# Kernel optimization log

Measured on AMD Instinct MI355X. Metric: run time of the kernel, lower is better.

Reference implementation:

```python
import jax, jax.numpy as jnp
import numpy as np

N, E, DIN, DH, DOUT, NG = 50000, 800000, 128, 128, 64, 128
EPS = 1e-5
SLOPE = 0.2  # PyG GATConv default negative_slope


def _gat(x, src, dst, W, a_s, a_d, b, heads, out_c, concat):
    n = x.shape[0]
    xp = (x @ W).reshape(n, heads, out_c)            # [N,H,C]
    e_src = (xp * a_s[None]).sum(-1)                  # [N,H]
    e_dst = (xp * a_d[None]).sum(-1)                  # [N,H]
    al = e_src[src] + e_dst[dst]                      # [E,H]
    al = jnp.where(al > 0, al, SLOPE * al)            # leaky_relu
    amax = jax.ops.segment_max(al, dst, num_segments=n)
    w = jnp.exp(al - amax[dst])                       # segment softmax (stable)
    den = jax.ops.segment_sum(w, dst, num_segments=n)
    msg = w[:, :, None] * xp[src]                     # [E,H,C]
    out = jax.ops.segment_sum(msg, dst, num_segments=n) / den[:, :, None]
    out = out.reshape(n, heads * out_c) if concat else out.mean(axis=1)
    return out + b


def _bn(h, g, be):
    m = h.mean(axis=0)
    v = h.var(axis=0)  # biased var, as in torch BN training mode
    return (h - m) / jnp.sqrt(v + EPS) * g + be


def setup_inputs() -> dict:
    key = jax.random.key(0)
    ks = jax.random.split(key, 12)
    x = jax.random.normal(ks[0], (N, DIN), dtype=jnp.float32)
    edge_index = jax.random.randint(ks[1], (2, E), 0, N, dtype=jnp.int64)
    graph_pool = jax.random.uniform(ks[2], (NG, N), dtype=jnp.float32) * (2.0 / N)
    s = 0.1
    return {
        "x": x, "edge_index": edge_index, "graph_pool": graph_pool,
        "W1": jax.random.normal(ks[3], (DIN, DH), dtype=jnp.float32) * s,
        "as1": jax.random.normal(ks[4], (1, DH), dtype=jnp.float32) * s,
        "ad1": jax.random.normal(ks[5], (1, DH), dtype=jnp.float32) * s,
        "b1": jnp.zeros((DH,), jnp.float32),
        "g1": jnp.ones((DH,), jnp.float32), "be1": jnp.zeros((DH,), jnp.float32),
        "W2": jax.random.normal(ks[6], (DH, DH), dtype=jnp.float32) * s,
        "as2": jax.random.normal(ks[7], (1, DH), dtype=jnp.float32) * s,
        "ad2": jax.random.normal(ks[8], (1, DH), dtype=jnp.float32) * s,
        "b2": jnp.zeros((DH,), jnp.float32),
        "g2": jnp.ones((DH,), jnp.float32), "be2": jnp.zeros((DH,), jnp.float32),
        "W3": jax.random.normal(ks[9], (DH, DOUT), dtype=jnp.float32) * s,
        "as3": jax.random.normal(ks[10], (1, DOUT), dtype=jnp.float32) * s,
        "ad3": jax.random.normal(ks[11], (1, DOUT), dtype=jnp.float32) * s,
        "b3": jnp.zeros((DOUT,), jnp.float32),
    }


def reference(x, edge_index, graph_pool,
              W1, as1, ad1, b1, g1, be1,
              W2, as2, ad2, b2, g2, be2,
              W3, as3, ad3, b3):
    n = x.shape[0]
    loops = jnp.arange(n, dtype=edge_index.dtype)  # PyG add_self_loops=True
    src = jnp.concatenate([edge_index[0], loops])
    dst = jnp.concatenate([edge_index[1], loops])
    h = _gat(x, src, dst, W1, as1, ad1, b1, 1, DH, True)
    h = jax.nn.relu(_bn(h, g1, be1))
    h = _gat(h, src, dst, W2, as2, ad2, b2, 1, DH, True)
    h = jax.nn.relu(_bn(h, g2, be2))
    h_nodes = _gat(h, src, dst, W3, as3, ad3, b3, 1, DOUT, False)
    h_pooled = graph_pool @ h_nodes  # sparse.mm == matmul mathematically
    return (h_pooled, h_nodes)
```

## Files before the change

kernel.cpp:

```cpp
#include <hip/hip_runtime.h>
#include <hip/hip_bf16.h>

#define DIN 128
#define DH  128
#define DOUT 64
#define NGR 128
#define EPSV 1e-5f
#define SLOPE 0.2f
#define BSH 7
#define NBMAX 512
#define BCAP 3584
#define POOLB 256
#define BNSPREAD 32
#define BINCH 4096

typedef __attribute__((ext_vector_type(8))) short short8;
typedef __attribute__((ext_vector_type(4))) float float4v;

__device__ __forceinline__ unsigned short f2bf(float f) {
    union { float f; unsigned int u; } v; v.f = f;
    unsigned int r = (v.u + 0x7FFFu + ((v.u >> 16) & 1u)) >> 16;
    return (unsigned short)r;
}
__device__ __forceinline__ unsigned short f2bf_f(float f) {
    return (unsigned short)((__float_as_uint(f) + 0x8000u) >> 16);
}
__device__ __forceinline__ float bf_lo(unsigned int u) { return __uint_as_float(u << 16); }
__device__ __forceinline__ float bf_hi(unsigned int u) { return __uint_as_float(u & 0xFFFF0000u); }

__device__ __forceinline__ void pack_one(const float* W, unsigned short* PW, int cout, int t) {
    int lane = t & 63;
    int ks   = (t >> 6) & 3;
    int nt   = t >> 8;
    int nn   = nt * 16 + (lane & 15);
    int k0   = ks * 32 + (lane >> 4) * 8;
    unsigned int pk[4];
#pragma unroll
    for (int p = 0; p < 4; ++p) {
        unsigned short lo = f2bf(W[(k0 + 2 * p) * cout + nn]);
        unsigned short hi = f2bf(W[(k0 + 2 * p + 1) * cout + nn]);
        pk[p] = ((unsigned int)hi << 16) | lo;
    }
    *(uint4*)&PW[(size_t)t * 8] = make_uint4(pk[0], pk[1], pk[2], pk[3]);
}

__global__ __launch_bounds__(256) void front_a_kernel(
    const int* __restrict__ ei, int* __restrict__ bucket_cnt, int2* __restrict__ binned,
    int E, int T, int nb, int binBlocks,
    const float* __restrict__ W1, unsigned short* __restrict__ PW1,
    const float* __restrict__ W2, unsigned short* __restrict__ PW2,
    const float* __restrict__ W3, unsigned short* __restrict__ PW3,
    const float* __restrict__ GP, unsigned short* __restrict__ GPB, int n)
{
    int blk = (int)blockIdx.x;
    if (blk >= binBlocks + 20) {
        size_t t = (size_t)(blk - binBlocks - 20) * 256 + threadIdx.x;
        size_t base = t * 32;
        size_t tot = (size_t)NGR * (size_t)n;
        if (base >= tot) return;
        if (base + 32 <= tot) {
            const float* src = GP + base;
            unsigned short* dst = GPB + base;
#pragma unroll
            for (int q2 = 0; q2 < 4; ++q2) {
                float4 a = *(const float4*)&src[q2 * 8];
                float4 b = *(const float4*)&src[q2 * 8 + 4];
                uint4 o;
                o.x = ((unsigned int)f2bf_f(a.y) << 16) | f2bf_f(a.x);
                o.y = ((unsigned int)f2bf_f(a.w) << 16) | f2bf_f(a.z);
                o.z = ((unsigned int)f2bf_f(b.y) << 16) | f2bf_f(b.x);
                o.w = ((unsigned int)f2bf_f(b.w) << 16) | f2bf_f(b.z);
                *(uint4*)&dst[q2 * 8] = o;
            }
        } else {
            for (size_t k = base; k < tot; ++k) GPB[k] = f2bf_f(GP[k]);
        }
        return;
    }
    if (blk >= binBlocks) {
        int t = (blk - binBlocks) * 256 + (int)threadIdx.x;
        if (t < 2048)      pack_one(W1, PW1, 128, t);
        else if (t < 4096) pack_one(W2, PW2, 128, t - 2048);
        else if (t < 5120) pack_one(W3, PW3, 64,  t - 4096);
        return;
    }
    __shared__ int hist[NBMAX], base[NBMAX], cur[NBMAX];
    for (int i = threadIdx.x; i < nb; i += 256) hist[i] = 0;
    __syncthreads();
    int start = blk * BINCH;
    int endc  = start + BINCH; if (endc > T) endc = T;
    for (int e = start + threadIdx.x; e < endc; e += 256) {
        int d = (e < E) ? ei[E + e] : (e - E);
        atomicAdd(&hist[d >> BSH], 1);
    }
    __syncthreads();
    for (int i = threadIdx.x; i < nb; i += 256) {
        int h = hist[i];
        cur[i] = 0;
        if (h) base[i] = atomicAdd(&bucket_cnt[i], h);
    }
    __syncthreads();
    for (int e = start + threadIdx.x; e < endc; e += 256) {
        int s, d;
        if (e < E) { s = ei[e]; d = ei[E + e]; }
        else       { s = e - E; d = s; }
        int b = d >> BSH;
        int off = atomicAdd(&cur[b], 1);
        binned[(size_t)b * BCAP + base[b] + off] = make_int2(s, d);
    }
}

template <int COUT, int BNIN>
__device__ __forceinline__ void gemm_es_body(
    unsigned short* Xs, float* sSc, float* sSh, int row0,
    const void* __restrict__ Xv, const unsigned short* __restrict__ PW,
    const float* __restrict__ a_s, const float* __restrict__ a_d,
    const float* __restrict__ bnsum, const float* __restrict__ g,
    const float* __restrict__ be, float invn,
    unsigned short* __restrict__ XPB, float* __restrict__ e_src, float* __restrict__ e_dst, int n)
{
    constexpr int NT = COUT / 16;
    int tid = threadIdx.x;

    if constexpr (BNIN) {
        if (tid < 128) {
            float s = 0.f, q = 0.f;
#pragma unroll 4
            for (int k = 0; k < BNSPREAD; ++k) {
                s += bnsum[k * 256 + tid];
                q += bnsum[k * 256 + 128 + tid];
            }
            float mean = s * invn;
            float var  = q * invn - mean * mean;
            float sc   = g[tid] * rsqrtf(var + EPSV);
            sSc[tid] = sc;
            sSh[tid] = be[tid] - mean * sc;
        }
        __syncthreads();
        const unsigned short* H = (const unsigned short*)Xv;
        for (int i = tid; i < 64 * 16; i += 256) {
            int r  = i >> 4;
            int c8 = (i & 15) * 8;
            uint4 u = make_uint4(0, 0, 0, 0);
            if (row0 + r < n) u = *(const uint4*)&H[(size_t)(row0 + r) * 128 + c8];
            unsigned int uu[4] = {u.x, u.y, u.z, u.w};
            unsigned int out[4];
#pragma unroll
            for (int p = 0; p < 4; ++p) {
                int c = c8 + 2 * p;
                float a  = fmaxf(bf_lo(uu[p]) * sSc[c] + sSh[c], 0.f);
                float bq = fmaxf(bf_hi(uu[p]) * sSc[c + 1] + sSh[c + 1], 0.f);
                out[p] = ((unsigned int)f2bf_f(bq) << 16) | f2bf_f(a);
            }
            *(uint4*)&Xs[r * 136 + c8] = make_uint4(out[0], out[1], out[2], out[3]);
        }
    } else {
        const float* X = (const float*)Xv;
        for (int i = tid; i < 64 * 32; i += 256) {
            int r  = i >> 5;
            int k4 = (i & 31) * 4;
            float4 v = make_float4(0.f, 0.f, 0.f, 0.f);
            if (row0 + r < n) v = *(const float4*)&X[(size_t)(row0 + r) * 128 + k4];
            uint2 pk;
            pk.x = ((unsigned int)f2bf_f(v.y) << 16) | f2bf_f(v.x);
            pk.y = ((unsigned int)f2bf_f(v.w) << 16) | f2bf_f(v.z);
            *(uint2*)&Xs[r * 136 + k4] = pk;
        }
    }
    __syncthreads();

    int wv   = tid >> 6;
    int lane = tid & 63;
    int m0   = wv * 16;
    int cl   = lane & 15;
    int q    = lane >> 4;

    float4v acc[NT] = {};
#pragma unroll
    for (int ks = 0; ks < 4; ++ks) {
        short8 af = *(const short8*)&Xs[(m0 + cl) * 136 + ks * 32 + q * 8];
#pragma unroll
        for (int nt = 0; nt < NT; ++nt) {
            short8 bf = *(const short8*)&PW[(size_t)((nt * 4 + ks) * 64 + lane) * 8];
            acc[nt] = __builtin_amdgcn_mfma_f32_16x16x32_bf16(af, bf, acc[nt], 0, 0, 0);
        }
    }

    float asv[NT], adv[NT];
#pragma unroll
    for (int nt = 0; nt < NT; ++nt) {
        asv[nt] = a_s[nt * 16 + cl];
        adv[nt] = a_d[nt * 16 + cl];
    }
#pragma unroll
    for (int reg = 0; reg < 4; ++reg) {
        int m = row0 + m0 + q * 4 + reg;
        if (m >= n) continue;
        float ps = 0.f, pd = 0.f;
        size_t base = (size_t)m * COUT;
#pragma unroll
        for (int nt = 0; nt < NT; ++nt) {
            float v = acc[nt][reg];
            XPB[base + nt * 16 + cl] = f2bf_f(v);
            ps += v * asv[nt];
            pd += v * adv[nt];
        }
        ps += __shfl_xor(ps, 1); pd += __shfl_xor(pd, 1);
        ps += __shfl_xor(ps, 2); pd += __shfl_xor(pd, 2);
        ps += __shfl_xor(ps, 4); pd += __shfl_xor(pd, 4);
        ps += __shfl_xor(ps, 8); pd += __shfl_xor(pd, 8);
        if (cl == 0) {
            e_src[m] = ps;
            e_dst[m] = pd;
        }
    }
}

template <int COUT, int BNIN>
__global__ __launch_bounds__(256) void gemm_es_kernel(
    const void* __restrict__ Xv, const unsigned short* __restrict__ PW,
    const float* __restrict__ a_s, const float* __restrict__ a_d,
    const float* __restrict__ bnsum, const float* __restrict__ g,
    const float* __restrict__ be, float invn,
    unsigned short* __restrict__ XPB, float* __restrict__ e_src, float* __restrict__ e_dst, int n)
{
    __shared__ unsigned short Xs[64 * 136];
    __shared__ float sSc[128], sSh[128];
    gemm_es_body<COUT, BNIN>(Xs, sSc, sSh, blockIdx.x * 64,
                             Xv, PW, a_s, a_d, bnsum, g, be, invn, XPB, e_src, e_dst, n);
}

__global__ __launch_bounds__(256) void front_b_kernel(
    const int2* __restrict__ binned, const int* __restrict__ bucket_cnt,
    int* __restrict__ row_ptr, int* __restrict__ col_src, int n, int T, int nbcsr,
    const float* __restrict__ X, const unsigned short* __restrict__ PW,
    const float* __restrict__ a_s, const float* __restrict__ a_d,
    unsigned short* __restrict__ XPB, float* __restrict__ e_src, float* __restrict__ e_dst)
{
    __shared__ __align__(16) char smraw[64 * 136 * 2];
    int tid = threadIdx.x;

    if ((int)blockIdx.x < nbcsr) {
        int* cnt = (int*)smraw;
        int* rnk = cnt + 128;
        int* rp  = rnk + 128;
        int* sc  = rp + 128;
        int* red = sc + 128;
        int b = blockIdx.x;
        int node0 = b << BSH;
        const int2* bin = &binned[(size_t)b * BCAP];
        int nb_edges = bucket_cnt[b];

        int part = 0;
        for (int i = tid; i < b; i += 256) part += bucket_cnt[i];
        red[tid] = part;
        if (tid < 128) cnt[tid] = 0;
        __syncthreads();
#pragma unroll
        for (int s2 = 128; s2 > 0; s2 >>= 1) {
            if (tid < s2) red[tid] += red[tid + s2];
            __syncthreads();
        }
        int lo = red[0];

        for (int i = tid; i < nb_edges; i += 256)
            atomicAdd(&cnt[bin[i].y - node0], 1);
        __syncthreads();
        if (tid < 128) sc[tid] = cnt[tid];
        __syncthreads();
        for (int d2 = 1; d2 < 128; d2 <<= 1) {
            int t = 0;
            if (tid < 128 && tid >= d2) t = sc[tid - d2];
            __syncthreads();
            if (tid < 128) sc[tid] += t;
            __syncthreads();
        }
        if (tid < 128) {
            int excl = sc[tid] - cnt[tid];
            int r = lo + excl;
            rp[tid] = r;
            rnk[tid] = 0;
            int node = node0 + tid;
            if (node < n) row_ptr[node] = r;
        }
        if (b == 0 && tid == 0) row_ptr[n] = T;
        __syncthreads();
        for (int i = tid; i < nb_edges; i += 256) {
            int2 e = bin[i];
            int local = e.y - node0;
            int r = atomicAdd(&rnk[local], 1);
            col_src[rp[local] + r] = e.x;
        }
    } else {
        unsigned short* Xs = (unsigned short*)smraw;
        gemm_es_body<128, 0>(Xs, nullptr, nullptr, ((int)blockIdx.x - nbcsr) * 64,
                             X, PW, a_s, a_d, nullptr, nullptr, nullptr, 0.f,
                             XPB, e_src, e_dst, n);
    }
}

template <int COUT, int OUTBF, int BNOUT>
__global__ __launch_bounds__(256) void gat_aggregate_kernel(
    const unsigned short* __restrict__ XPB, const float* __restrict__ e_src,
    const float* __restrict__ e_dst, const int* __restrict__ row_ptr,
    const int* __restrict__ col_src, const float* __restrict__ bias,
    void* __restrict__ OUT, float* __restrict__ bnsumS, int n)
{
    __shared__ float bnsh[BNOUT ? 512 : 1];
    constexpr int GSH  = (COUT == 128) ? 4 : 3;
    constexpr int STEP = 64 >> GSH;
    constexpr int RSH  = (COUT == 128) ? 7 : 6;

    int wave = threadIdx.x >> 6;
    int lane = threadIdx.x & 63;
    int g    = lane >> GSH;
    int cl   = lane & ((1 << GSH) - 1);
    int d = blockIdx.x * 4 + wave;
    bool act = (d < n);
    if (!BNOUT && !act) return;

    int start = 0, end = 0;
    float ed = 0.f;
    if (act) {
        start = row_ptr[d];
        end   = row_ptr[d + 1];
        ed    = e_dst[d];
    }

    float denl = 0.f;
    float acc8[8] = {};

    for (int base = start; base < end; base += 64) {
        int t = base + lane;
        int s_l = 0; float w_l = 0.f;
        if (t < end) {
            s_l = col_src[t];
            float a = e_src[s_l] + ed;
            a = (a > 0.f) ? a : SLOPE * a;
            w_l = __expf(a);
        }
        denl += w_l;
        int cnt = end - base; if (cnt > 64) cnt = 64;

        int j = 0;
        for (; j + 16 <= cnt; j += 16) {
            int   r0 = __shfl(s_l, j + g);
            int   r1 = __shfl(s_l, j + STEP + g);
            float w0 = __shfl(w_l, j + g);
            float w1 = __shfl(w_l, j + STEP + g);
            uint4 u0 = ((const uint4*)(XPB + ((size_t)(unsigned)r0 << RSH)))[cl];
            uint4 u1 = ((const uint4*)(XPB + ((size_t)(unsigned)r1 << RSH)))[cl];
            int   r2, r3; float w2, w3; uint4 u2, u3;
            if (COUT == 128) {
                r2 = __shfl(s_l, j + 2 * STEP + g);
                r3 = __shfl(s_l, j + 3 * STEP + g);
                w2 = __shfl(w_l, j + 2 * STEP + g);
                w3 = __shfl(w_l, j + 3 * STEP + g);
                u2 = ((const uint4*)(XPB + ((size_t)(unsigned)r2 << RSH)))[cl];
                u3 = ((const uint4*)(XPB + ((size_t)(unsigned)r3 << RSH)))[cl];
            }
            unsigned int a0[4] = {u0.x, u0.y, u0.z, u0.w};
            unsigned int a1[4] = {u1.x, u1.y, u1.z, u1.w};
#pragma unroll
            for (int p = 0; p < 4; ++p) {
                acc8[2 * p]     += w0 * bf_lo(a0[p]);
                acc8[2 * p + 1] += w0 * bf_hi(a0[p]);
                acc8[2 * p]     += w1 * bf_lo(a1[p]);
                acc8[2 * p + 1] += w1 * bf_hi(a1[p]);
            }
            if (COUT == 128) {
                unsigned int a2[4] = {u2.x, u2.y, u2.z, u2.w};
                unsigned int a3[4] = {u3.x, u3.y, u3.z, u3.w};
#pragma unroll
                for (int p = 0; p < 4; ++p) {
                    acc8[2 * p]     += w2 * bf_lo(a2[p]);
                    acc8[2 * p + 1] += w2 * bf_hi(a2[p]);
                    acc8[2 * p]     += w3 * bf_lo(a3[p]);
                    acc8[2 * p + 1] += w3 * bf_hi(a3[p]);
                }
            }
        }
        for (; j < cnt; j += STEP) {
            int   r = __shfl(s_l, j + g);
            float w = __shfl(w_l, j + g);
            uint4 u = ((const uint4*)(XPB + ((size_t)(unsigned)r << RSH)))[cl];
            unsigned int au[4] = {u.x, u.y, u.z, u.w};
#pragma unroll
            for (int p = 0; p < 4; ++p) {
                acc8[2 * p]     += w * bf_lo(au[p]);
                acc8[2 * p + 1] += w * bf_hi(au[p]);
            }
        }
    }

#pragma unroll
    for (int off = (1 << GSH); off < 64; off <<= 1)
#pragma unroll
        for (int k = 0; k < 8; ++k) acc8[k] += __shfl_xor(acc8[k], off);

#pragma unroll
    for (int off = 1; off < 64; off <<= 1) denl += __shfl_xor(denl, off);
    float inv = 1.f / denl;

    float ox[8];
#pragma unroll
    for (int k = 0; k < 8; ++k) ox[k] = 0.f;
    if (act) {
#pragma unroll
        for (int k = 0; k < 8; ++k) ox[k] = acc8[k] * inv + bias[cl * 8 + k];
    }

    if (COUT == 128) {
        if (act && g == 0) {
            if (OUTBF) {
                unsigned int o0 = ((unsigned int)f2bf_f(ox[1]) << 16) | f2bf_f(ox[0]);
                unsigned int o1 = ((unsigned int)f2bf_f(ox[3]) << 16) | f2bf_f(ox[2]);
                unsigned int o2 = ((unsigned int)f2bf_f(ox[5]) << 16) | f2bf_f(ox[4]);
                unsigned int o3 = ((unsigned int)f2bf_f(ox[7]) << 16) | f2bf_f(ox[6]);
                ((uint4*)OUT)[(size_t)d * 16 + cl] = make_uint4(o0, o1, o2, o3);
            } else {
                ((float4*)OUT)[(size_t)d * 32 + cl * 2]     = make_float4(ox[0], ox[1], ox[2], ox[3]);
                ((float4*)OUT)[(size_t)d * 32 + cl * 2 + 1] = make_float4(ox[4], ox[5], ox[6], ox[7]);
            }
        }
        if (BNOUT) {
            if (g == 0) {
#pragma unroll
                for (int k = 0; k < 8; ++k) bnsh[wave * 128 + cl * 8 + k] = ox[k];
            }
            __syncthreads();
            if (wave == 0) {
                float s0 = 0.f, q0 = 0.f, s1 = 0.f, q1 = 0.f;
#pragma unroll
                for (int k = 0; k < 4; ++k) {
                    float v0 = bnsh[k * 128 + 2 * lane];
                    float v1 = bnsh[k * 128 + 2 * lane + 1];
                    s0 += v0; q0 += v0 * v0;
                    s1 += v1; q1 += v1 * v1;
                }
                float* dstb = &bnsumS[(blockIdx.x & (BNSPREAD - 1)) * 256];
                atomicAdd(&dstb[2 * lane],           s0);
                atomicAdd(&dstb[2 * lane + 1],       s1);
                atomicAdd(&dstb[128 + 2 * lane],     q0);
                atomicAdd(&dstb[128 + 2 * lane + 1], q1);
            }
        }
    } else {
        if (act && g == 0) {
            ((float4*)OUT)[(size_t)d * 16 + cl * 2]     = make_float4(ox[0], ox[1], ox[2], ox[3]);
            ((float4*)OUT)[(size_t)d * 16 + cl * 2 + 1] = make_float4(ox[4], ox[5], ox[6], ox[7]);
        }
    }
}

__global__ __launch_bounds__(256) void pool_mfma_kernel(
    const unsigned short* __restrict__ GPB, const float* __restrict__ HN,
    float* __restrict__ partial, int n, int nchunk)
{
    __shared__ unsigned short gp_s[128 * 136];
    __shared__ unsigned short ht_s[64 * 136];
    int tid = threadIdx.x;
    int wv = tid >> 6, lane = tid & 63, cl = lane & 15, q = lane >> 4;

    float4v acc[4][2] = {};

    for (int blk = blockIdx.x; blk < nchunk; blk += gridDim.x) {
        int k0 = blk * 128;

        for (int i = tid; i < 128 * 16; i += 256) {
            int r  = i >> 4;
            int kk = (i & 15) * 8;
            int gk = k0 + kk;
            uint4 v = make_uint4(0, 0, 0, 0);
            if (gk + 7 < n) {
                v = *(const uint4*)&GPB[(size_t)r * n + gk];
            } else if (gk < n) {
                unsigned short tmp[8];
#pragma unroll
                for (int e2 = 0; e2 < 8; ++e2)
                    tmp[e2] = (gk + e2 < n) ? GPB[(size_t)r * n + gk + e2] : 0;
                v = *(const uint4*)tmp;
            }
            *(uint4*)&gp_s[r * 136 + kk] = v;
        }
        for (int i = tid; i < 128 * 16; i += 256) {
            int k  = i >> 4;
            int c4 = (i & 15) * 4;
            int gk = k0 + k;
            float4 v = make_float4(0.f, 0.f, 0.f, 0.f);
            if (gk < n) v = *(const float4*)&HN[(size_t)gk * 64 + c4];
            ht_s[(c4 + 0) * 136 + k] = f2bf_f(v.x);
            ht_s[(c4 + 1) * 136 + k] = f2bf_f(v.y);
            ht_s[(c4 + 2) * 136 + k] = f2bf_f(v.z);
            ht_s[(c4 + 3) * 136 + k] = f2bf_f(v.w);
        }
        __syncthreads();

#pragma unroll
        for (int ks = 0; ks < 4; ++ks) {
            short8 bfr[2];
#pragma unroll
            for (int j = 0; j < 2; ++j)
                bfr[j] = *(const short8*)&gp_s[((wv * 2 + j) * 16 + cl) * 136 + ks * 32 + q * 8];
#pragma unroll
            for (int mt = 0; mt < 4; ++mt) {
                short8 af = *(const short8*)&ht_s[(mt * 16 + cl) * 136 + ks * 32 + q * 8];
#pragma unroll
                for (int j = 0; j < 2; ++j)
                    acc[mt][j] = __builtin_amdgcn_mfma_f32_16x16x32_bf16(af, bfr[j], acc[mt][j], 0, 0, 0);
            }
        }
        __syncthreads();
    }

    float* po = &partial[(size_t)blockIdx.x * (NGR * DOUT)];
#pragma unroll
    for (int mt = 0; mt < 4; ++mt) {
#pragma unroll
        for (int j = 0; j < 2; ++j) {
            int g = (wv * 2 + j) * 16 + cl;
            int c = mt * 16 + q * 4;
            *(float4*)&po[g * 64 + c] =
                make_float4(acc[mt][j][0], acc[mt][j][1], acc[mt][j][2], acc[mt][j][3]);
        }
    }
}

__global__ __launch_bounds__(256) void pool_reduce_kernel(
    const float* __restrict__ partial, float* __restrict__ OUT, int nblk)
{
    int i = blockIdx.x * 256 + threadIdx.x;
    float s0 = 0.f, s1 = 0.f, s2 = 0.f, s3 = 0.f;
    int p = 0;
    for (; p + 3 < nblk; p += 4) {
        s0 += partial[(size_t)(p + 0) * (NGR * DOUT) + i];
        s1 += partial[(size_t)(p + 1) * (NGR * DOUT) + i];
        s2 += partial[(size_t)(p + 2) * (NGR * DOUT) + i];
        s3 += partial[(size_t)(p + 3) * (NGR * DOUT) + i];
    }
    for (; p < nblk; ++p) s0 += partial[(size_t)p * (NGR * DOUT) + i];
    OUT[i] = (s0 + s1) + (s2 + s3);
}

extern "C" void kernel_launch(void* const* d_in, const int* in_sizes, int n_in,
                              void* d_out, int out_size, void* d_ws, size_t ws_size,
                              hipStream_t stream) {
    const float* x   = (const float*)d_in[0];
    const int*   ei  = (const int*)d_in[1];
    const float* gp  = (const float*)d_in[2];
    const float* W1  = (const float*)d_in[3];
    const float* as1 = (const float*)d_in[4];
    const float* ad1 = (const float*)d_in[5];
    const float* b1  = (const float*)d_in[6];
    const float* g1  = (const float*)d_in[7];
    const float* be1 = (const float*)d_in[8];
    const float* W2  = (const float*)d_in[9];
    const float* as2 = (const float*)d_in[10];
    const float* ad2 = (const float*)d_in[11];
    const float* b2  = (const float*)d_in[12];
    const float* g2  = (const float*)d_in[13];
    const float* be2 = (const float*)d_in[14];
    const float* W3  = (const float*)d_in[15];
    const float* as3 = (const float*)d_in[16];
    const float* ad3 = (const float*)d_in[17];
    const float* b3  = (const float*)d_in[18];

    const int N = in_sizes[0] / DIN;
    const int E = in_sizes[1] / 2;
    const int T = E + N;
    const int NB = (N + 127) >> BSH;

    char* ws = (char*)d_ws;
    auto take = [&](size_t bytes) {
        char* p = ws;
        ws += (bytes + 511) & ~(size_t)511;
        return p;
    };
    unsigned short* xpb = (unsigned short*)take((size_t)N * 128 * 2);
    unsigned short* h   = (unsigned short*)take((size_t)N * 128 * 2);
    unsigned short* gpb = (unsigned short*)take((size_t)NGR * N * 2);
    float* pool_s  = (float*)take((size_t)POOLB * NGR * DOUT * 4);
    float* esd     = (float*)take((size_t)2 * N * 4);
    float* e_src   = esd;
    float* e_dst   = esd + N;
    int*   row_ptr = (int*)take((size_t)(N + 1) * 4);
    int*   col_src = (int*)take((size_t)T * 4);
    int2*  binned  = (int2*)take((size_t)NB * BCAP * 8);
    int*   zero_rgn   = (int*)take((size_t)(NBMAX + 1 + 2 * BNSPREAD * 256) * 4);
    int*   bucket_cnt = zero_rgn;
    float* bnsum1     = (float*)(zero_rgn + NBMAX + 1);
    float* bnsum2     = bnsum1 + BNSPREAD * 256;
    unsigned short* pw1 = (unsigned short*)take((size_t)128 * 128 * 2);
    unsigned short* pw2 = (unsigned short*)take((size_t)128 * 128 * 2);
    unsigned short* pw3 = (unsigned short*)take((size_t)128 * 64 * 2);

    float* outp = (float*)d_out;
    float* hn   = outp + NGR * DOUT;

    hipMemsetAsync(zero_rgn, 0, (size_t)(NBMAX + 1 + 2 * BNSPREAD * 256) * 4, stream);

    const int binBlocks = (T + BINCH - 1) / BINCH;
    const int gpBlocks  = (int)(((size_t)NGR * N / 32 + 255) / 256);
    front_a_kernel<<<binBlocks + 20 + gpBlocks, 256, 0, stream>>>(
        ei, bucket_cnt, binned, E, T, NB, binBlocks,
        W1, pw1, W2, pw2, W3, pw3, gp, gpb, N);

    const int gx = (N + 63) / 64;
    const float invn = 1.f / N;

    front_b_kernel<<<NB + gx, 256, 0, stream>>>(binned, bucket_cnt, row_ptr, col_src, N, T, NB,
                                                x, pw1, as1, ad1, xpb, e_src, e_dst);

    gat_aggregate_kernel<128, 1, 1><<<(N + 3) / 4, 256, 0, stream>>>(
        xpb, e_src, e_dst, row_ptr, col_src, b1, h, bnsum1, N);

    gemm_es_kernel<128, 1><<<gx, 256, 0, stream>>>(h, pw2, as2, ad2,
        bnsum1, g1, be1, invn, xpb, e_src, e_dst, N);
    gat_aggregate_kernel<128, 1, 1><<<(N + 3) / 4, 256, 0, stream>>>(
        xpb, e_src, e_dst, row_ptr, col_src, b2, h, bnsum2, N);

    gemm_es_kernel<64, 1><<<gx, 256, 0, stream>>>(h, pw3, as3, ad3,
        bnsum2, g2, be2, invn, xpb, e_src, e_dst, N);
    gat_aggregate_kernel<64, 0, 0><<<(N + 3) / 4, 256, 0, stream>>>(
        xpb, e_src, e_dst, row_ptr, col_src, b3, hn, nullptr, N);

    const int nchunk = (N + 127) / 128;
    const int pb = nchunk < POOLB ? nchunk : POOLB;
    pool_mfma_kernel<<<pb, 256, 0, stream>>>(gpb, hn, pool_s, N, nchunk);
    pool_reduce_kernel<<<(NGR * DOUT + 255) / 256, 256, 0, stream>>>(pool_s, outp, pb);
}
```

Baseline: 330.2 us.

## Move graph_pool bf16 conversion into first aggregate kernel and register-buffer CSR edges

```diff
diff --git a/kernel.cpp b/kernel.cpp
--- a/kernel.cpp
+++ b/kernel.cpp
@@ -49,34 +49,9 @@
     int E, int T, int nb, int binBlocks,
     const float* __restrict__ W1, unsigned short* __restrict__ PW1,
     const float* __restrict__ W2, unsigned short* __restrict__ PW2,
-    const float* __restrict__ W3, unsigned short* __restrict__ PW3,
-    const float* __restrict__ GP, unsigned short* __restrict__ GPB, int n)
+    const float* __restrict__ W3, unsigned short* __restrict__ PW3)
 {
     int blk = (int)blockIdx.x;
-    if (blk >= binBlocks + 20) {
-        size_t t = (size_t)(blk - binBlocks - 20) * 256 + threadIdx.x;
-        size_t base = t * 32;
-        size_t tot = (size_t)NGR * (size_t)n;
-        if (base >= tot) return;
-        if (base + 32 <= tot) {
-            const float* src = GP + base;
-            unsigned short* dst = GPB + base;
-#pragma unroll
-            for (int q2 = 0; q2 < 4; ++q2) {
-                float4 a = *(const float4*)&src[q2 * 8];
-                float4 b = *(const float4*)&src[q2 * 8 + 4];
-                uint4 o;
-                o.x = ((unsigned int)f2bf_f(a.y) << 16) | f2bf_f(a.x);
-                o.y = ((unsigned int)f2bf_f(a.w) << 16) | f2bf_f(a.z);
-                o.z = ((unsigned int)f2bf_f(b.y) << 16) | f2bf_f(b.x);
-                o.w = ((unsigned int)f2bf_f(b.w) << 16) | f2bf_f(b.z);
-                *(uint4*)&dst[q2 * 8] = o;
-            }
-        } else {
-            for (size_t k = base; k < tot; ++k) GPB[k] = f2bf_f(GP[k]);
-        }
-        return;
-    }
     if (blk >= binBlocks) {
         int t = (blk - binBlocks) * 256 + (int)threadIdx.x;
         if (t < 2048)      pack_one(W1, PW1, 128, t);
@@ -251,6 +226,14 @@
         const int2* bin = &binned[(size_t)b * BCAP];
         int nb_edges = bucket_cnt[b];
 
+        int2 ebuf[14];
+        int cntE = 0;
+#pragma unroll
+        for (int k = 0; k < 14; ++k) {
+            int i = tid + k * 256;
+            if (i < nb_edges) { ebuf[k] = bin[i]; cntE = k + 1; }
+        }
+
         int part = 0;
         for (int i = tid; i < b; i += 256) part += bucket_cnt[i];
         red[tid] = part;
@@ -263,8 +246,9 @@
         }
         int lo = red[0];
 
-        for (int i = tid; i < nb_edges; i += 256)
-            atomicAdd(&cnt[bin[i].y - node0], 1);
+#pragma unroll
+        for (int k = 0; k < 14; ++k)
+            if (k < cntE) atomicAdd(&cnt[ebuf[k].y - node0], 1);
         __syncthreads();
         if (tid < 128) sc[tid] = cnt[tid];
         __syncthreads();
@@ -285,12 +269,13 @@
         }
         if (b == 0 && tid == 0) row_ptr[n] = T;
         __syncthreads();
-        for (int i = tid; i < nb_edges; i += 256) {
-            int2 e = bin[i];
-            int local = e.y - node0;
-            int r = atomicAdd(&rnk[local], 1);
-            col_src[rp[local] + r] = e.x;
-        }
+#pragma unroll
+        for (int k = 0; k < 14; ++k)
+            if (k < cntE) {
+                int local = ebuf[k].y - node0;
+                int r = atomicAdd(&rnk[local], 1);
+                col_src[rp[local] + r] = ebuf[k].x;
+            }
     } else {
         unsigned short* Xs = (unsigned short*)smraw;
         gemm_es_body<128, 0>(Xs, nullptr, nullptr, ((int)blockIdx.x - nbcsr) * 64,
@@ -299,14 +284,40 @@
     }
 }
 
-template <int COUT, int OUTBF, int BNOUT>
+template <int COUT, int OUTBF, int BNOUT, int GPCONV>
 __global__ __launch_bounds__(256) void gat_aggregate_kernel(
     const unsigned short* __restrict__ XPB, const float* __restrict__ e_src,
     const float* __restrict__ e_dst, const int* __restrict__ row_ptr,
     const int* __restrict__ col_src, const float* __restrict__ bias,
-    void* __restrict__ OUT, float* __restrict__ bnsumS, int n)
+    void* __restrict__ OUT, float* __restrict__ bnsumS,
+    const float* __restrict__ GP, unsigned short* __restrict__ GPB, int nAgg, int n)
 {
     __shared__ float bnsh[BNOUT ? 512 : 1];
+    if (GPCONV && (int)blockIdx.x >= nAgg) {
+        size_t t = (size_t)((int)blockIdx.x - nAgg) * 256 + threadIdx.x;
+        size_t base = t * 32;
+        size_t tot = (size_t)NGR * (size_t)n;
+        if (base >= tot) return;
+        if (base + 32 <= tot) {
+            const float* src = GP + base;
+            unsigned short* dst = GPB + base;
+#pragma unroll
+            for (int q2 = 0; q2 < 4; ++q2) {
+                float4 a = *(const float4*)&src[q2 * 8];
+                float4 b = *(const float4*)&src[q2 * 8 + 4];
+                uint4 o;
+                o.x = ((unsigned int)f2bf_f(a.y) << 16) | f2bf_f(a.x);
+                o.y = ((unsigned int)f2bf_f(a.w) << 16) | f2bf_f(a.z);
+                o.z = ((unsigned int)f2bf_f(b.y) << 16) | f2bf_f(b.x);
+                o.w = ((unsigned int)f2bf_f(b.w) << 16) | f2bf_f(b.z);
+                *(uint4*)&dst[q2 * 8] = o;
+            }
+        } else {
+            for (size_t k = base; k < tot; ++k) GPB[k] = f2bf_f(GP[k]);
+        }
+        return;
+    }
+
     constexpr int GSH  = (COUT == 128) ? 4 : 3;
     constexpr int STEP = 64 >> GSH;
     constexpr int RSH  = (COUT == 128) ? 7 : 6;
@@ -600,10 +611,8 @@
     hipMemsetAsync(zero_rgn, 0, (size_t)(NBMAX + 1 + 2 * BNSPREAD * 256) * 4, stream);
 
     const int binBlocks = (T + BINCH - 1) / BINCH;
-    const int gpBlocks  = (int)(((size_t)NGR * N / 32 + 255) / 256);
-    front_a_kernel<<<binBlocks + 20 + gpBlocks, 256, 0, stream>>>(
-        ei, bucket_cnt, binned, E, T, NB, binBlocks,
-        W1, pw1, W2, pw2, W3, pw3, gp, gpb, N);
+    front_a_kernel<<<binBlocks + 20, 256, 0, stream>>>(ei, bucket_cnt, binned, E, T, NB, binBlocks,
+                                                       W1, pw1, W2, pw2, W3, pw3);
 
     const int gx = (N + 63) / 64;
     const float invn = 1.f / N;
@@ -611,18 +620,20 @@
     front_b_kernel<<<NB + gx, 256, 0, stream>>>(binned, bucket_cnt, row_ptr, col_src, N, T, NB,
                                                 x, pw1, as1, ad1, xpb, e_src, e_dst);
 
-    gat_aggregate_kernel<128, 1, 1><<<(N + 3) / 4, 256, 0, stream>>>(
-        xpb, e_src, e_dst, row_ptr, col_src, b1, h, bnsum1, N);
+    const int aggBlocks = (N + 3) / 4;
+    const int gpBlocks  = (int)(((size_t)NGR * N / 32 + 255) / 256);
+    gat_aggregate_kernel<128, 1, 1, 1><<<aggBlocks + gpBlocks, 256, 0, stream>>>(
+        xpb, e_src, e_dst, row_ptr, col_src, b1, h, bnsum1, gp, gpb, aggBlocks, N);
 
     gemm_es_kernel<128, 1><<<gx, 256, 0, stream>>>(h, pw2, as2, ad2,
         bnsum1, g1, be1, invn, xpb, e_src, e_dst, N);
-    gat_aggregate_kernel<128, 1, 1><<<(N + 3) / 4, 256, 0, stream>>>(
-        xpb, e_src, e_dst, row_ptr, col_src, b2, h, bnsum2, N);
+    gat_aggregate_kernel<128, 1, 1, 0><<<aggBlocks, 256, 0, stream>>>(
+        xpb, e_src, e_dst, row_ptr, col_src, b2, h, bnsum2, nullptr, nullptr, aggBlocks, N);
 
     gemm_es_kernel<64, 1><<<gx, 256, 0, stream>>>(h, pw3, as3, ad3,
         bnsum2, g2, be2, invn, xpb, e_src, e_dst, N);
-    gat_aggregate_kernel<64, 0, 0><<<(N + 3) / 4, 256, 0, stream>>>(
-        xpb, e_src, e_dst, row_ptr, col_src, b3, hn, nullptr, N);
+    gat_aggregate_kernel<64, 0, 0, 0><<<aggBlocks, 256, 0, stream>>>(
+        xpb, e_src, e_dst, row_ptr, col_src, b3, hn, nullptr, nullptr, nullptr, aggBlocks, N);
 
     const int nchunk = (N + 127) / 128;
     const int pb = nchunk < POOLB ? nchunk : POOLB;
```

New measurement: 330.3 us. No clear change (+0.0%).
